# Kernel optimization log

Hardware: AMD Instinct MI355X
Metric: run time of the kernel (lower is better)

The kernel has to match this reference:

```python
import jax, jax.numpy as jnp
import numpy as np

D_MODEL = 1024
H = 16
D_K = D_MODEL // H
NEG_INF = -1.0e9  # matches masked_fill value in the torch source


def setup_inputs() -> dict:
    key = jax.random.key(0)
    kq, kk, kv, kwq, kwk, kwv, kwo = jax.random.split(key, 7)
    B, S = 2, 2048
    query = jax.random.normal(kq, (B, S, D_MODEL), dtype=jnp.float32)
    key_t = jax.random.normal(kk, (B, S, D_MODEL), dtype=jnp.float32)
    value = jax.random.normal(kv, (B, S, D_MODEL), dtype=jnp.float32)
    # causal mask: 1 = attend, 0 = masked (masked_fill(mask == 0, -1e9))
    masked_val = jnp.tril(jnp.ones((S, S), dtype=jnp.int32))[None, None, :, :]
    scale = 1.0 / np.sqrt(D_MODEL)
    w_q = jax.random.normal(kwq, (D_MODEL, D_MODEL), dtype=jnp.float32) * scale
    w_k = jax.random.normal(kwk, (D_MODEL, D_MODEL), dtype=jnp.float32) * scale
    w_v = jax.random.normal(kwv, (D_MODEL, D_MODEL), dtype=jnp.float32) * scale
    w_o = jax.random.normal(kwo, (D_MODEL, D_MODEL), dtype=jnp.float32) * scale
    return {"query": query, "key": key_t, "value": value, "masked_val": masked_val,
            "w_q": w_q, "w_k": w_k, "w_v": w_v, "w_o": w_o}


def reference(query, key, value, masked_val, w_q, w_k, w_v, w_o):
    B, Sq, _ = query.shape
    Sk = key.shape[1]
    # nn.Linear(x) = x @ W.T; weights stored as [out, in]
    Q = (query @ w_q.T).reshape(B, Sq, H, D_K).transpose(0, 2, 1, 3)  # [B,H,Sq,Dk]
    K = (key @ w_k.T).reshape(B, Sk, H, D_K).transpose(0, 2, 1, 3)    # [B,H,Sk,Dk]
    V = (value @ w_v.T).reshape(B, Sk, H, D_K).transpose(0, 2, 1, 3)  # [B,H,Sk,Dk]
    scores = jnp.einsum("bhqd,bhkd->bhqk", Q, K) / jnp.sqrt(jnp.float32(D_K))
    scores = jnp.where(masked_val == 0, NEG_INF, scores)
    probs = jax.nn.softmax(scores, axis=-1)  # dropout p=0.0 -> identity
    ctx = jnp.einsum("bhqk,bhkd->bhqd", probs, V)  # [B,H,Sq,Dk]
    ctx = ctx.transpose(0, 2, 1, 3).reshape(B, Sq, H * D_K)
    return ctx @ w_o.T
```

## Files before the change

kernel.cpp:

```cpp
#include <hip/hip_runtime.h>
#include <hip/hip_bf16.h>
#include <type_traits>

using bf16x8_t = __attribute__((ext_vector_type(8))) __bf16;
using f32x4_t  = __attribute__((ext_vector_type(4))) float;

#define MFMA16(a, b, c) __builtin_amdgcn_mfma_f32_16x16x32_bf16((a), (b), (c), 0, 0, 0)

constexpr int BATCH   = 2;
constexpr int SEQ     = 2048;
constexpr int DMODEL  = 1024;
constexpr int DK      = 64;
constexpr int MTOT    = BATCH * SEQ;
constexpr float SCL2 = 0.125f * 1.44269504088896f;

typedef const __attribute__((address_space(1))) unsigned int ga_u32;
typedef __attribute__((address_space(3))) unsigned int ls_u32;
__device__ __forceinline__ void glds16(const void* g, void* l) {
    __builtin_amdgcn_global_load_lds((ga_u32*)g, (ls_u32*)l, 16, 0, 0);
}

__device__ __forceinline__ float exp2_fast(float x) {
    float r;
    asm volatile("v_exp_f32 %0, %1" : "=v"(r) : "v"(x));
    return r;
}

__device__ __forceinline__ bf16x8_t cvt8(const float* __restrict__ p) {
    f32x4_t a = *(const f32x4_t*)p;
    f32x4_t b = *(const f32x4_t*)(p + 4);
    bf16x8_t r;
    r[0] = (__bf16)a[0]; r[1] = (__bf16)a[1]; r[2] = (__bf16)a[2]; r[3] = (__bf16)a[3];
    r[4] = (__bf16)b[0]; r[5] = (__bf16)b[1]; r[6] = (__bf16)b[2]; r[7] = (__bf16)b[3];
    return r;
}

__device__ __forceinline__ bf16x8_t pack_row_frag(const float* row_base, int row, int lhi) {
    f32x4_t v0 = *(const f32x4_t*)(row_base + ((lhi * 2 + 0) ^ (row & 7)) * 4);
    f32x4_t v1 = *(const f32x4_t*)(row_base + ((lhi * 2 + 1) ^ (row & 7)) * 4);
    bf16x8_t r;
    r[0] = (__bf16)v0[0]; r[1] = (__bf16)v0[1]; r[2] = (__bf16)v0[2]; r[3] = (__bf16)v0[3];
    r[4] = (__bf16)v1[0]; r[5] = (__bf16)v1[1]; r[6] = (__bf16)v1[2]; r[7] = (__bf16)v1[3];
    return r;
}

__global__ __launch_bounds__(256) void cvt_w_kernel(
    const float* __restrict__ w0, const float* __restrict__ w1,
    const float* __restrict__ w2, const float* __restrict__ w3, __bf16* __restrict__ dst)
{
    const float* srcs[4] = {w0, w1, w2, w3};
    const float* s = srcs[blockIdx.y];
    __bf16* d = dst + (size_t)blockIdx.y * (DMODEL * DMODEL);
    size_t i = ((size_t)blockIdx.x * 256 + threadIdx.x) * 8;
    *(bf16x8_t*)(d + i) = cvt8(s + i);
}

template<bool A_BF16, bool C_F32>
__device__ __forceinline__ void gemm_body(
    const void* __restrict__ Ap, const __bf16* __restrict__ Bt,
    void* __restrict__ Cp, int m0, int n0)
{
    constexpr int K = DMODEL, N = DMODEL;
    constexpr int A_LS_BYTES = A_BF16 ? 8192 : 16384;
    constexpr int BUF_BYTES  = A_LS_BYTES + 8192;
    __shared__ __align__(16) char smem[2][BUF_BYTES];

    const int tid  = threadIdx.x;
    const int wave = tid >> 6, lane = tid & 63;
    const int wm = wave >> 1, wn = wave & 1;
    const int l15 = lane & 15, lhi = lane >> 4;

    auto stage = [&](int k0, int buf) {
        char* a_ls = smem[buf];
        char* b_ls = smem[buf] + A_LS_BYTES;
        if constexpr (A_BF16) {
            const __bf16* Ab = (const __bf16*)Ap;
            #pragma unroll
            for (int i = 0; i < 2; ++i) {
                int cbase = i * 256 + wave * 64;
                int slot = cbase + lane;
                int row = slot >> 2, c = slot & 3;
                int cs = (c + 4 - ((row >> 1) & 3)) & 3;
                glds16(Ab + (size_t)(m0 + row) * K + k0 + cs * 8, a_ls + (size_t)cbase * 16);
            }
        } else {
            const float* Af = (const float*)Ap;
            #pragma unroll
            for (int i = 0; i < 4; ++i) {
                int cbase = i * 256 + wave * 64;
                int slot = cbase + lane;
                int row = slot >> 3, c = (slot & 7) ^ (row & 7);
                glds16(Af + (size_t)(m0 + row) * K + k0 + c * 4, a_ls + (size_t)cbase * 16);
            }
        }
        #pragma unroll
        for (int i = 0; i < 2; ++i) {
            int cbase = i * 256 + wave * 64;
            int slot = cbase + lane;
            int row = slot >> 2, c = slot & 3;
            int cs = (c + 4 - ((row >> 1) & 3)) & 3;
            glds16(Bt + (size_t)(n0 + row) * K + k0 + cs * 8, b_ls + (size_t)cbase * 16);
        }
    };

    f32x4_t acc[4][4] = {};
    stage(0, 0);
    __syncthreads();

    for (int st = 0; st < K / 32; ++st) {
        if (st < K / 32 - 1) stage((st + 1) * 32, (st + 1) & 1);

        const char*   a_ls = smem[st & 1];
        const __bf16* b_ls = (const __bf16*)(smem[st & 1] + A_LS_BYTES);

        bf16x8_t af[4], bfr[4];
        #pragma unroll
        for (int i = 0; i < 4; ++i) {
            int row = wm * 64 + i * 16 + l15;
            if constexpr (A_BF16) {
                int lc = (lhi + (row >> 1)) & 3;
                af[i] = *(const bf16x8_t*)((const __bf16*)a_ls + row * 32 + lc * 8);
            } else {
                af[i] = pack_row_frag((const float*)a_ls + row * 32, row, lhi);
            }
        }
        #pragma unroll
        for (int j = 0; j < 4; ++j) {
            int row = wn * 64 + j * 16 + l15;
            int lc = (lhi + (row >> 1)) & 3;
            bfr[j] = *(const bf16x8_t*)(b_ls + row * 32 + lc * 8);
        }
        #pragma unroll
        for (int i = 0; i < 4; ++i)
            #pragma unroll
            for (int j = 0; j < 4; ++j)
                acc[i][j] = MFMA16(af[i], bfr[j], acc[i][j]);

        __syncthreads();
    }

    #pragma unroll
    for (int i = 0; i < 4; ++i)
        #pragma unroll
        for (int j = 0; j < 4; ++j)
            #pragma unroll
            for (int r = 0; r < 4; ++r) {
                int row = m0 + wm * 64 + i * 16 + lhi * 4 + r;
                int col = n0 + wn * 64 + j * 16 + l15;
                if constexpr (C_F32)
                    ((float*)Cp)[(size_t)row * N + col] = acc[i][j][r];
                else
                    ((__bf16*)Cp)[(size_t)row * N + col] = (__bf16)acc[i][j][r];
            }
}

__global__ __launch_bounds__(256) void proj_qkv_kernel(
    const float* __restrict__ xq, const float* __restrict__ xk, const float* __restrict__ xv,
    const __bf16* __restrict__ wc,
    __bf16* __restrict__ oq, __bf16* __restrict__ ok, __bf16* __restrict__ ov)
{
    int lid = blockIdx.x + 8 * blockIdx.y + 256 * blockIdx.z;
    int nid = (lid & 7) * 96 + (lid >> 3);
    int z = nid >> 8, rem = nid & 255;
    int m0 = (rem >> 3) * 128, n0 = (rem & 7) * 128;

    const float* A; const __bf16* Bt; __bf16* C;
    if (z == 0)      { A = xq; Bt = wc;                       C = oq; }
    else if (z == 1) { A = xk; Bt = wc + DMODEL * DMODEL;     C = ok; }
    else             { A = xv; Bt = wc + 2 * DMODEL * DMODEL; C = ov; }
    gemm_body<false, false>(A, Bt, C, m0, n0);
}

__global__ __launch_bounds__(256) void proj_out_kernel(
    const __bf16* __restrict__ ctx, const __bf16* __restrict__ woc, float* __restrict__ out)
{
    int lid = blockIdx.x + 8 * blockIdx.y;
    int nid = (lid & 7) * 32 + (lid >> 3);
    gemm_body<true, true>(ctx, woc, out, (nid >> 3) * 128, (nid & 7) * 128);
}

__global__ __launch_bounds__(256, 4) void attn_kernel(
    const __bf16* __restrict__ Qm, const __bf16* __restrict__ Km,
    const __bf16* __restrict__ Vm, __bf16* __restrict__ Om)
{
    constexpr int LDV = 72, LDP = 72;
    __shared__ __bf16 k_sh[2][64 * 64];
    __shared__ __bf16 v_sh[64 * LDV];
    __shared__ __bf16 p_sh[4][16 * LDP];

    const int tid  = threadIdx.x;
    const int wave = tid >> 6, lane = tid & 63;
    const int l15 = lane & 15, lhi = lane >> 4;

    int old = blockIdx.x + 32 * blockIdx.y;
    int nid = (old & 7) * 128 + (old >> 3);
    const int x = nid & 31, y = nid >> 5;
    const int p = (y & 1) ? 31 - x : x;
    const int q0 = p * 64;
    const int b = y >> 4, h = y & 15;

    const __bf16* Qb = Qm + (size_t)b * SEQ * DMODEL + h * DK;
    const __bf16* Kb = Km + (size_t)b * SEQ * DMODEL + h * DK;
    const __bf16* Vb = Vm + (size_t)b * SEQ * DMODEL + h * DK;

    const int qbase = q0 + wave * 16;

    bf16x8_t qf[2];
    {
        const __bf16* qp = Qb + (size_t)(qbase + l15) * DMODEL + lhi * 8;
        qf[0] = *(const bf16x8_t*)qp;
        qf[1] = *(const bf16x8_t*)(qp + 32);
    }

    f32x4_t acc[4] = {};
    float m2[4] = {-INFINITY, -INFINITY, -INFINITY, -INFINITY};
    float lsum[4] = {0.f, 0.f, 0.f, 0.f};

    const int vrow = tid >> 3, vgrp = tid & 7;
    bf16x8_t vreg0, vreg1;

    auto stageK = [&](int kv0, int buf) {
        #pragma unroll
        for (int i = 0; i < 2; ++i) {
            int cbase = i * 256 + wave * 64;
            int slot = cbase + lane;
            int row = slot >> 3, c = (slot & 7) ^ (row & 7);
            glds16(Kb + (size_t)(kv0 + row) * DMODEL + c * 8,
                   (char*)k_sh[buf] + (size_t)cbase * 16);
        }
    };
    auto loadV = [&](int kv0) {
        vreg0 = *(const bf16x8_t*)(Vb + (size_t)(kv0 + vrow) * DMODEL + vgrp * 8);
        vreg1 = *(const bf16x8_t*)(Vb + (size_t)(kv0 + 32 + vrow) * DMODEL + vgrp * 8);
    };
    auto writeV = [&]() {
        int sh0 = (vrow + vgrp * 8) & 63;
        #pragma unroll
        for (int j = 0; j < 8; ++j) v_sh[(vgrp * 8 + j) * LDV + sh0] = vreg0[j];
        int sh1 = (vrow + 32 + vgrp * 8) & 63;
        #pragma unroll
        for (int j = 0; j < 8; ++j) v_sh[(vgrp * 8 + j) * LDV + sh1] = vreg1[j];
    };

    auto body = [&](auto needmask_c, int kv0, int cur) {
        constexpr bool NEEDMASK = decltype(needmask_c)::value;
        const __bf16* ks_buf = k_sh[cur];

        f32x4_t sf[4] = {};
        #pragma unroll
        for (int ks = 0; ks < 2; ++ks)
            #pragma unroll
            for (int n = 0; n < 4; ++n) {
                int row = n * 16 + l15;
                bf16x8_t kf = *(const bf16x8_t*)(ks_buf + row * 64 + (((ks * 4 + lhi) ^ (row & 7)) * 8));
                sf[n] = MFMA16(qf[ks], kf, sf[n]);
            }

        const int qrow_base = qbase + lhi * 4;
        float pmax[4];
        #pragma unroll
        for (int r = 0; r < 4; ++r) {
            float mx = -3.0e38f;
            #pragma unroll
            for (int n = 0; n < 4; ++n) {
                float sv = sf[n][r] * SCL2;
                if constexpr (NEEDMASK)
                    if (kv0 + n * 16 + l15 > qrow_base + r) sv = -1.0e30f;
                sf[n][r] = sv;
                mx = fmaxf(mx, sv);
            }
            pmax[r] = mx;
        }
        #pragma unroll
        for (int r = 0; r < 4; ++r)
            #pragma unroll
            for (int off = 1; off < 16; off <<= 1)
                pmax[r] = fmaxf(pmax[r], __shfl_xor(pmax[r], off, 64));

        bool grew = (pmax[0] > m2[0]) || (pmax[1] > m2[1]) ||
                    (pmax[2] > m2[2]) || (pmax[3] > m2[3]);
        if (__any((int)grew)) {
            #pragma unroll
            for (int r = 0; r < 4; ++r) {
                float mnew = fmaxf(m2[r], pmax[r]);
                float sfac = exp2_fast(m2[r] - mnew);
                m2[r] = mnew;
                lsum[r] *= sfac;
                #pragma unroll
                for (int n = 0; n < 4; ++n) acc[n][r] *= sfac;
            }
        }

        #pragma unroll
        for (int r = 0; r < 4; ++r) {
            float rs = 0.f;
            #pragma unroll
            for (int n = 0; n < 4; ++n) {
                float pv = exp2_fast(sf[n][r] - m2[r]);
                sf[n][r] = pv;
                rs += pv;
            }
            lsum[r] += rs;
        }

        #pragma unroll
        for (int r = 0; r < 4; ++r)
            #pragma unroll
            for (int n = 0; n < 4; ++n)
                p_sh[wave][(lhi * 4 + r) * LDP + ((n * 16 + l15 + ((lhi >> 1) << 3)) & 63)]
                    = (__bf16)sf[n][r];

        #pragma unroll
        for (int ks = 0; ks < 2; ++ks) {
            bf16x8_t pa = *(const bf16x8_t*)(
                &p_sh[wave][l15 * LDP + ((ks * 32 + lhi * 8 + ((l15 >> 3) << 3)) & 63)]);
            #pragma unroll
            for (int n = 0; n < 4; ++n) {
                int d = n * 16 + l15;
                int rot = (ks * 32 + lhi * 8 + ((d >> 3) << 3)) & 63;
                bf16x8_t vf = *(const bf16x8_t*)(v_sh + d * LDV + rot);
                acc[n] = MFMA16(pa, vf, acc[n]);
            }
        }
    };

    stageK(0, 0);
    loadV(0);
    __syncthreads();
    writeV();
    __syncthreads();

    for (int t = 0; t < p; ++t) {
        int cur = t & 1;
        stageK((t + 1) * 64, cur ^ 1);
        loadV((t + 1) * 64);
        body(std::integral_constant<bool, false>{}, t * 64, cur);
        __syncthreads();
        writeV();
        __syncthreads();
    }
    body(std::integral_constant<bool, true>{}, p * 64, p & 1);

    #pragma unroll
    for (int r = 0; r < 4; ++r) {
        #pragma unroll
        for (int off = 1; off < 16; off <<= 1)
            lsum[r] += __shfl_xor(lsum[r], off, 64);
    }
    __bf16* Ob = Om + (size_t)b * SEQ * DMODEL + h * DK;
    #pragma unroll
    for (int n = 0; n < 4; ++n)
        #pragma unroll
        for (int r = 0; r < 4; ++r) {
            int row = qbase + lhi * 4 + r;
            Ob[(size_t)row * DMODEL + n * 16 + l15] = (__bf16)(acc[n][r] / lsum[r]);
        }
}

extern "C" void kernel_launch(void* const* d_in, const int* in_sizes, int n_in,
                              void* d_out, int out_size, void* d_ws, size_t ws_size,
                              hipStream_t stream)
{
    const float* q  = (const float*)d_in[0];
    const float* k  = (const float*)d_in[1];
    const float* v  = (const float*)d_in[2];
    const float* wq = (const float*)d_in[4];
    const float* wk = (const float*)d_in[5];
    const float* wv = (const float*)d_in[6];
    const float* wo = (const float*)d_in[7];
    float* out = (float*)d_out;

    const size_t mat = (size_t)MTOT * DMODEL;
    __bf16* Qw = (__bf16*)d_ws;
    __bf16* Kw = Qw + mat;
    __bf16* Vw = Kw + mat;
    __bf16* Cw = Vw + mat;
    __bf16* Wc = Cw + mat;

    dim3 blk(256);
    cvt_w_kernel<<<dim3(512, 4), blk, 0, stream>>>(wq, wk, wv, wo, Wc);
    proj_qkv_kernel<<<dim3(8, 32, 3), blk, 0, stream>>>(q, k, v, Wc, Qw, Kw, Vw);
    attn_kernel<<<dim3(32, 32), blk, 0, stream>>>(Qw, Kw, Vw, Cw);
    proj_out_kernel<<<dim3(8, 32), blk, 0, stream>>>(Cw, Wc + 3 * DMODEL * DMODEL, out);
}
```

Baseline: 136.7 us.

## Convert fp32 A to bf16 in registers, fold softmax scale, MFMA row sums, lazy rescale

The QKV projection now loads fp32 activations into registers and writes them to LDS as bf16, which halves the LDS tile size and replaces the per-fragment fp32 unpack. The softmax scale is folded into the Q projection epilogue, so the per-score multiply in attention goes away. Row sums of P are computed with an MFMA against a ones vector instead of VALU adds and shuffles. Rescaling of the running max is skipped unless the max grows by more than 8 in log2 units, trading exact max tracking for fewer rescale passes at a small risk of overflow in the exponentials.

```diff
diff --git a/kernel.cpp b/kernel.cpp
--- a/kernel.cpp
+++ b/kernel.cpp
@@ -3,6 +3,7 @@
 #include <type_traits>
 
 using bf16x8_t = __attribute__((ext_vector_type(8))) __bf16;
+using bf16x4_t = __attribute__((ext_vector_type(4))) __bf16;
 using f32x4_t  = __attribute__((ext_vector_type(4))) float;
 
 #define MFMA16(a, b, c) __builtin_amdgcn_mfma_f32_16x16x32_bf16((a), (b), (c), 0, 0, 0)
@@ -35,15 +36,6 @@
     return r;
 }
 
-__device__ __forceinline__ bf16x8_t pack_row_frag(const float* row_base, int row, int lhi) {
-    f32x4_t v0 = *(const f32x4_t*)(row_base + ((lhi * 2 + 0) ^ (row & 7)) * 4);
-    f32x4_t v1 = *(const f32x4_t*)(row_base + ((lhi * 2 + 1) ^ (row & 7)) * 4);
-    bf16x8_t r;
-    r[0] = (__bf16)v0[0]; r[1] = (__bf16)v0[1]; r[2] = (__bf16)v0[2]; r[3] = (__bf16)v0[3];
-    r[4] = (__bf16)v1[0]; r[5] = (__bf16)v1[1]; r[6] = (__bf16)v1[2]; r[7] = (__bf16)v1[3];
-    return r;
-}
-
 __global__ __launch_bounds__(256) void cvt_w_kernel(
     const float* __restrict__ w0, const float* __restrict__ w1,
     const float* __restrict__ w2, const float* __restrict__ w3, __bf16* __restrict__ dst)
@@ -58,71 +50,92 @@
 template<bool A_BF16, bool C_F32>
 __device__ __forceinline__ void gemm_body(
     const void* __restrict__ Ap, const __bf16* __restrict__ Bt,
-    void* __restrict__ Cp, int m0, int n0)
+    void* __restrict__ Cp, int m0, int n0, float cscale)
 {
     constexpr int K = DMODEL, N = DMODEL;
-    constexpr int A_LS_BYTES = A_BF16 ? 8192 : 16384;
-    constexpr int BUF_BYTES  = A_LS_BYTES + 8192;
-    __shared__ __align__(16) char smem[2][BUF_BYTES];
+    constexpr int NSTEPS = K / 32;
+    __shared__ __align__(16) char smem[2][16384];
 
     const int tid  = threadIdx.x;
     const int wave = tid >> 6, lane = tid & 63;
     const int wm = wave >> 1, wn = wave & 1;
     const int l15 = lane & 15, lhi = lane >> 4;
 
-    auto stage = [&](int k0, int buf) {
-        char* a_ls = smem[buf];
-        char* b_ls = smem[buf] + A_LS_BYTES;
-        if constexpr (A_BF16) {
-            const __bf16* Ab = (const __bf16*)Ap;
-            #pragma unroll
-            for (int i = 0; i < 2; ++i) {
-                int cbase = i * 256 + wave * 64;
-                int slot = cbase + lane;
-                int row = slot >> 2, c = slot & 3;
-                int cs = (c + 4 - ((row >> 1) & 3)) & 3;
-                glds16(Ab + (size_t)(m0 + row) * K + k0 + cs * 8, a_ls + (size_t)cbase * 16);
-            }
-        } else {
-            const float* Af = (const float*)Ap;
-            #pragma unroll
-            for (int i = 0; i < 4; ++i) {
-                int cbase = i * 256 + wave * 64;
-                int slot = cbase + lane;
-                int row = slot >> 3, c = (slot & 7) ^ (row & 7);
-                glds16(Af + (size_t)(m0 + row) * K + k0 + c * 4, a_ls + (size_t)cbase * 16);
-            }
-        }
+    auto glds_A_bf16 = [&](int k0, int buf) {
+        const __bf16* Ab = (const __bf16*)Ap;
         #pragma unroll
         for (int i = 0; i < 2; ++i) {
             int cbase = i * 256 + wave * 64;
             int slot = cbase + lane;
             int row = slot >> 2, c = slot & 3;
             int cs = (c + 4 - ((row >> 1) & 3)) & 3;
-            glds16(Bt + (size_t)(n0 + row) * K + k0 + cs * 8, b_ls + (size_t)cbase * 16);
+            glds16(Ab + (size_t)(m0 + row) * K + k0 + cs * 8, smem[buf] + (size_t)cbase * 16);
+        }
+    };
+    auto glds_B = [&](int k0, int buf) {
+        #pragma unroll
+        for (int i = 0; i < 2; ++i) {
+            int cbase = i * 256 + wave * 64;
+            int slot = cbase + lane;
+            int row = slot >> 2, c = slot & 3;
+            int cs = (c + 4 - ((row >> 1) & 3)) & 3;
+            glds16(Bt + (size_t)(n0 + row) * K + k0 + cs * 8,
+                   smem[buf] + 8192 + (size_t)cbase * 16);
+        }
+    };
+    auto load_A_f32 = [&](int k0, f32x4_t (&ar)[4]) {
+        const float* Af = (const float*)Ap;
+        #pragma unroll
+        for (int i = 0; i < 4; ++i) {
+            int g = i * 256 + tid;
+            int row = g >> 3, c = g & 7;
+            ar[i] = *(const f32x4_t*)(Af + (size_t)(m0 + row) * K + k0 + c * 4);
+        }
+    };
+    auto write_A_f32 = [&](const f32x4_t (&ar)[4], int buf) {
+        __bf16* a_ls = (__bf16*)smem[buf];
+        #pragma unroll
+        for (int i = 0; i < 4; ++i) {
+            int g = i * 256 + tid;
+            int row = g >> 3, c = g & 7;
+            int pc = ((c >> 1) + ((row >> 1) & 3)) & 3;
+            bf16x4_t w;
+            w[0] = (__bf16)ar[i][0]; w[1] = (__bf16)ar[i][1];
+            w[2] = (__bf16)ar[i][2]; w[3] = (__bf16)ar[i][3];
+            *(bf16x4_t*)(a_ls + row * 32 + pc * 8 + (c & 1) * 4) = w;
         }
     };
 
     f32x4_t acc[4][4] = {};
-    stage(0, 0);
+
+    {
+        f32x4_t ar0[4];
+        if constexpr (A_BF16) glds_A_bf16(0, 0);
+        else                  load_A_f32(0, ar0);
+        glds_B(0, 0);
+        if constexpr (!A_BF16) write_A_f32(ar0, 0);
+    }
     __syncthreads();
 
-    for (int st = 0; st < K / 32; ++st) {
-        if (st < K / 32 - 1) stage((st + 1) * 32, (st + 1) & 1);
-
-        const char*   a_ls = smem[st & 1];
-        const __bf16* b_ls = (const __bf16*)(smem[st & 1] + A_LS_BYTES);
-
+    for (int st = 0; st < NSTEPS; ++st) {
+        const int cur = st & 1;
+        const bool have_next = (st + 1 < NSTEPS);
+        f32x4_t areg[4];
+        if (have_next) {
+            const int k1 = (st + 1) * 32;
+            if constexpr (A_BF16) glds_A_bf16(k1, cur ^ 1);
+            else                  load_A_f32(k1, areg);
+            glds_B(k1, cur ^ 1);
+        }
+
+        const __bf16* a_ls = (const __bf16*)smem[cur];
+        const __bf16* b_ls = (const __bf16*)(smem[cur] + 8192);
         bf16x8_t af[4], bfr[4];
         #pragma unroll
         for (int i = 0; i < 4; ++i) {
             int row = wm * 64 + i * 16 + l15;
-            if constexpr (A_BF16) {
-                int lc = (lhi + (row >> 1)) & 3;
-                af[i] = *(const bf16x8_t*)((const __bf16*)a_ls + row * 32 + lc * 8);
-            } else {
-                af[i] = pack_row_frag((const float*)a_ls + row * 32, row, lhi);
-            }
+            int lc = (lhi + (row >> 1)) & 3;
+            af[i] = *(const bf16x8_t*)(a_ls + row * 32 + lc * 8);
         }
         #pragma unroll
         for (int j = 0; j < 4; ++j) {
@@ -136,7 +149,10 @@
             for (int j = 0; j < 4; ++j)
                 acc[i][j] = MFMA16(af[i], bfr[j], acc[i][j]);
 
-        __syncthreads();
+        if (have_next) {
+            if constexpr (!A_BF16) write_A_f32(areg, cur ^ 1);
+            __syncthreads();
+        }
     }
 
     #pragma unroll
@@ -147,10 +163,11 @@
             for (int r = 0; r < 4; ++r) {
                 int row = m0 + wm * 64 + i * 16 + lhi * 4 + r;
                 int col = n0 + wn * 64 + j * 16 + l15;
+                float v = acc[i][j][r] * cscale;
                 if constexpr (C_F32)
-                    ((float*)Cp)[(size_t)row * N + col] = acc[i][j][r];
+                    ((float*)Cp)[(size_t)row * N + col] = v;
                 else
-                    ((__bf16*)Cp)[(size_t)row * N + col] = (__bf16)acc[i][j][r];
+                    ((__bf16*)Cp)[(size_t)row * N + col] = (__bf16)v;
             }
 }
 
@@ -164,11 +181,11 @@
     int z = nid >> 8, rem = nid & 255;
     int m0 = (rem >> 3) * 128, n0 = (rem & 7) * 128;
 
-    const float* A; const __bf16* Bt; __bf16* C;
-    if (z == 0)      { A = xq; Bt = wc;                       C = oq; }
-    else if (z == 1) { A = xk; Bt = wc + DMODEL * DMODEL;     C = ok; }
-    else             { A = xv; Bt = wc + 2 * DMODEL * DMODEL; C = ov; }
-    gemm_body<false, false>(A, Bt, C, m0, n0);
+    const float* A; const __bf16* Bt; __bf16* C; float cs;
+    if (z == 0)      { A = xq; Bt = wc;                       C = oq; cs = SCL2; }
+    else if (z == 1) { A = xk; Bt = wc + DMODEL * DMODEL;     C = ok; cs = 1.0f; }
+    else             { A = xv; Bt = wc + 2 * DMODEL * DMODEL; C = ov; cs = 1.0f; }
+    gemm_body<false, false>(A, Bt, C, m0, n0, cs);
 }
 
 __global__ __launch_bounds__(256) void proj_out_kernel(
@@ -176,7 +193,7 @@
 {
     int lid = blockIdx.x + 8 * blockIdx.y;
     int nid = (lid & 7) * 32 + (lid >> 3);
-    gemm_body<true, true>(ctx, woc, out, (nid >> 3) * 128, (nid & 7) * 128);
+    gemm_body<true, true>(ctx, woc, out, (nid >> 3) * 128, (nid & 7) * 128, 1.0f);
 }
 
 __global__ __launch_bounds__(256, 4) void attn_kernel(
@@ -211,10 +228,13 @@
         qf[0] = *(const bf16x8_t*)qp;
         qf[1] = *(const bf16x8_t*)(qp + 32);
     }
+    bf16x8_t onesf;
+    #pragma unroll
+    for (int j = 0; j < 8; ++j) onesf[j] = (__bf16)1.0f;
 
     f32x4_t acc[4] = {};
+    f32x4_t acc_l = {};
     float m2[4] = {-INFINITY, -INFINITY, -INFINITY, -INFINITY};
-    float lsum[4] = {0.f, 0.f, 0.f, 0.f};
 
     const int vrow = tid >> 3, vgrp = tid & 7;
     bf16x8_t vreg0, vreg1;
@@ -263,7 +283,7 @@
             float mx = -3.0e38f;
             #pragma unroll
             for (int n = 0; n < 4; ++n) {
-                float sv = sf[n][r] * SCL2;
+                float sv = sf[n][r];
                 if constexpr (NEEDMASK)
                     if (kv0 + n * 16 + l15 > qrow_base + r) sv = -1.0e30f;
                 sf[n][r] = sv;
@@ -277,31 +297,25 @@
             for (int off = 1; off < 16; off <<= 1)
                 pmax[r] = fmaxf(pmax[r], __shfl_xor(pmax[r], off, 64));
 
-        bool grew = (pmax[0] > m2[0]) || (pmax[1] > m2[1]) ||
-                    (pmax[2] > m2[2]) || (pmax[3] > m2[3]);
+        bool grew = (pmax[0] > m2[0] + 8.f) || (pmax[1] > m2[1] + 8.f) ||
+                    (pmax[2] > m2[2] + 8.f) || (pmax[3] > m2[3] + 8.f);
         if (__any((int)grew)) {
             #pragma unroll
             for (int r = 0; r < 4; ++r) {
                 float mnew = fmaxf(m2[r], pmax[r]);
                 float sfac = exp2_fast(m2[r] - mnew);
                 m2[r] = mnew;
-                lsum[r] *= sfac;
+                acc_l[r] *= sfac;
                 #pragma unroll
                 for (int n = 0; n < 4; ++n) acc[n][r] *= sfac;
             }
         }
 
         #pragma unroll
-        for (int r = 0; r < 4; ++r) {
-            float rs = 0.f;
-            #pragma unroll
-            for (int n = 0; n < 4; ++n) {
-                float pv = exp2_fast(sf[n][r] - m2[r]);
-                sf[n][r] = pv;
-                rs += pv;
-            }
-            lsum[r] += rs;
-        }
+        for (int r = 0; r < 4; ++r)
+            #pragma unroll
+            for (int n = 0; n < 4; ++n)
+                sf[n][r] = exp2_fast(sf[n][r] - m2[r]);
 
         #pragma unroll
         for (int r = 0; r < 4; ++r)
@@ -314,6 +328,7 @@
         for (int ks = 0; ks < 2; ++ks) {
             bf16x8_t pa = *(const bf16x8_t*)(
                 &p_sh[wave][l15 * LDP + ((ks * 32 + lhi * 8 + ((l15 >> 3) << 3)) & 63)]);
+            acc_l = MFMA16(pa, onesf, acc_l);
             #pragma unroll
             for (int n = 0; n < 4; ++n) {
                 int d = n * 16 + l15;
@@ -341,19 +356,13 @@
     }
     body(std::integral_constant<bool, true>{}, p * 64, p & 1);
 
-    #pragma unroll
-    for (int r = 0; r < 4; ++r) {
-        #pragma unroll
-        for (int off = 1; off < 16; off <<= 1)
-            lsum[r] += __shfl_xor(lsum[r], off, 64);
-    }
     __bf16* Ob = Om + (size_t)b * SEQ * DMODEL + h * DK;
     #pragma unroll
     for (int n = 0; n < 4; ++n)
         #pragma unroll
         for (int r = 0; r < 4; ++r) {
             int row = qbase + lhi * 4 + r;
-            Ob[(size_t)row * DMODEL + n * 16 + l15] = (__bf16)(acc[n][r] / lsum[r]);
+            Ob[(size_t)row * DMODEL + n * 16 + l15] = (__bf16)(acc[n][r] / acc_l[r]);
         }
 }
 
```

Result: faster. 129.7 us (-5.1%).
